# Performance work log

Hardware: AMD Instinct MI355X
Metric: run time of the kernel (lower is better)

Reference implementation:

```python
import jax, jax.numpy as jnp
import numpy as np

N, IN_DIM, H, L, NH, LAT = 4096, 16, 128, 4, 8, 16
HD = H // NH
FF = 2 * H
DR_THR = 0.2
LN_EPS = 1e-5


def _ln(x, s, b):
    m = x.mean(-1, keepdims=True)
    v = ((x - m) ** 2).mean(-1, keepdims=True)
    return (x - m) * jax.lax.rsqrt(v + LN_EPS) * s + b


def compute_dr_mask(x_raw):
    eta = x_raw[:, 1] * (2.62 - (-2.62)) + (-2.62)
    phi = x_raw[:, 2] * (3.1416 - (-3.1416)) + (-3.1416)
    deta = eta[:, None] - eta[None, :]
    dphi = phi[:, None] - phi[None, :]
    dphi = jnp.arctan2(jnp.sin(dphi), jnp.cos(dphi))
    dr = jnp.sqrt(deta ** 2 + dphi ** 2)
    return jnp.where(dr <= DR_THR, 0.0, -jnp.inf).astype(jnp.float32)


def setup_inputs() -> dict:
    key = jax.random.key(0)
    ks = jax.random.split(key, 32)
    g = lambda i, shape, s=0.02: (jax.random.normal(ks[i], shape, dtype=jnp.float32) * s)
    inp = {
        'x_raw': jax.random.uniform(ks[0], (N, IN_DIM), dtype=jnp.float32),
        'batch': jnp.zeros((N,), dtype=jnp.int64) if jax.config.read('jax_enable_x64') else jnp.zeros((N,), dtype=jnp.int32),
        'in_w': g(1, (H, IN_DIM), 0.1), 'in_b': jnp.zeros((H,), jnp.float32),
        'ln1_s': jnp.ones((L, H), jnp.float32), 'ln1_b': jnp.zeros((L, H), jnp.float32),
        'qkv_w': g(2, (L, 3 * H, H)), 'qkv_b': jnp.zeros((L, 3 * H), jnp.float32),
        'ao_w': g(3, (L, H, H)), 'ao_b': jnp.zeros((L, H), jnp.float32),
        'ln2_s': jnp.ones((L, H), jnp.float32), 'ln2_b': jnp.zeros((L, H), jnp.float32),
        'f1_w': g(4, (L, FF, H)), 'f1_b': jnp.zeros((L, FF), jnp.float32),
        'f2_w': g(5, (L, H, FF)), 'f2_b': jnp.zeros((L, H), jnp.float32),
        'lat1_w': g(6, (H, H), 0.08), 'lat1_b': jnp.zeros((H,), jnp.float32),
        'lat2_w': g(7, (LAT, H), 0.08), 'lat2_b': jnp.zeros((LAT,), jnp.float32),
        'b1_w': g(8, (H // 2, H), 0.08), 'b1_b': jnp.zeros((H // 2,), jnp.float32),
        'b2_w': g(9, (1, H // 2), 0.008), 'b2_b': jnp.full((1,), -3.0, jnp.float32),
    }
    return inp


def reference(x_raw, batch, in_w, in_b, ln1_s, ln1_b, qkv_w, qkv_b, ao_w, ao_b,
              ln2_s, ln2_b, f1_w, f1_b, f2_w, f2_b,
              lat1_w, lat1_b, lat2_w, lat2_b, b1_w, b1_b, b2_w, b2_b):
    mask = jax.lax.stop_gradient(compute_dr_mask(x_raw))  # [N, N] additive mask
    x = x_raw @ in_w.T + in_b  # [N, H]
    scale = 1.0 / jnp.sqrt(jnp.float32(HD))
    for l in range(L):  # norm_first TransformerEncoderLayer, eval mode (no dropout)
        h = _ln(x, ln1_s[l], ln1_b[l])
        qkv = h @ qkv_w[l].T + qkv_b[l]
        q, k, v = [t.reshape(N, NH, HD) for t in jnp.split(qkv, 3, axis=-1)]
        scores = jnp.einsum('qhd,khd->hqk', q, k) * scale + mask[None]
        attn = jax.nn.softmax(scores, axis=-1)
        o = jnp.einsum('hqk,khd->qhd', attn, v).reshape(N, H)
        x = x + o @ ao_w[l].T + ao_b[l]
        h2 = _ln(x, ln2_s[l], ln2_b[l])
        x = x + jax.nn.relu(h2 @ f1_w[l].T + f1_b[l]) @ f2_w[l].T + f2_b[l]
    lat = jax.nn.relu(x @ lat1_w.T + lat1_b) @ lat2_w.T + lat2_b  # [N, LAT]
    lat = lat / jnp.maximum(jnp.linalg.norm(lat, axis=-1, keepdims=True), 1e-12)
    beta = jax.nn.sigmoid(jax.nn.relu(x @ b1_w.T + b1_b) @ b2_w.T + b2_b)
    beta = jnp.clip(beta, 1e-6, 1 - 1e-6)  # [N, 1]
    return beta, lat
```

## Files before the change

kernel.cpp:

```cpp
#include <hip/hip_runtime.h>
#include <hip/hip_bf16.h>

typedef unsigned short u16;
typedef short short8_t __attribute__((ext_vector_type(8)));
typedef float floatx4 __attribute__((ext_vector_type(4)));

constexpr int NT = 4096, H = 128, CAP = 64;
constexpr int GRID = 256, BLK = 512, GSTRIDE = GRID * BLK;
constexpr int NGRP = 8, GRPSZ = GRID / NGRP;

constexpr int OFF_QKV  = 0;
constexpr int OFF_AO   = 196608;
constexpr int OFF_F1   = 262144;
constexpr int OFF_F2   = 393216;
constexpr int OFF_LAT1 = 524288;
constexpr int OFF_B1   = 540672;
constexpr int OFF_LAT2 = 548864;
constexpr int W_TOTAL  = 550912;

__device__ __forceinline__ float bfu(u16 u) { return __uint_as_float(((unsigned)u) << 16); }
__device__ __forceinline__ u16 f2bf(float f) {
  unsigned u = __float_as_uint(f);
  u += 0x7fffu + ((u >> 16) & 1u);
  return (u16)(u >> 16);
}
__device__ __forceinline__ void unpack8(uint4 u, float* f) {
  f[0] = __uint_as_float(u.x << 16); f[1] = __uint_as_float(u.x & 0xffff0000u);
  f[2] = __uint_as_float(u.y << 16); f[3] = __uint_as_float(u.y & 0xffff0000u);
  f[4] = __uint_as_float(u.z << 16); f[5] = __uint_as_float(u.z & 0xffff0000u);
  f[6] = __uint_as_float(u.w << 16); f[7] = __uint_as_float(u.w & 0xffff0000u);
}
__device__ __forceinline__ short8_t cvt8(const float* bp) {
  const float4 f0 = *(const float4*)bp, f1 = *(const float4*)(bp + 4);
  short8_t r;
  r[0] = (short)f2bf(f0.x); r[1] = (short)f2bf(f0.y);
  r[2] = (short)f2bf(f0.z); r[3] = (short)f2bf(f0.w);
  r[4] = (short)f2bf(f1.x); r[5] = (short)f2bf(f1.y);
  r[6] = (short)f2bf(f1.z); r[7] = (short)f2bf(f1.w);
  return r;
}

__device__ __forceinline__ void st64(unsigned long long* p, unsigned long long v) {
  __hip_atomic_store(p, v, __ATOMIC_RELAXED, __HIP_MEMORY_SCOPE_AGENT);
}
__device__ __forceinline__ void st16(u16* p, u16 v) {
  __hip_atomic_store(p, v, __ATOMIC_RELAXED, __HIP_MEMORY_SCOPE_AGENT);
}

__device__ __forceinline__ void gridbar(int* bar, int grp, int e) {
  __syncthreads();
  if (threadIdx.x == 0) {
    asm volatile("" ::: "memory");
    int* root = bar;
    int* gcnt = bar + 16 + 16 * grp;
    const int old = __hip_atomic_fetch_add(gcnt, 1, __ATOMIC_RELAXED,
                                           __HIP_MEMORY_SCOPE_AGENT);
    if (old == GRPSZ * e - 1)
      __hip_atomic_fetch_add(root, 1, __ATOMIC_RELAXED, __HIP_MEMORY_SCOPE_AGENT);
    while (__hip_atomic_load(root, __ATOMIC_RELAXED, __HIP_MEMORY_SCOPE_AGENT) < NGRP * e)
      __builtin_amdgcn_s_sleep(2);
    asm volatile("" ::: "memory");
  }
  __syncthreads();
}

struct Prm {
  const float *xr, *in_w, *in_b, *ln1_s, *ln1_b, *qkv_w, *qkv_b, *ao_w, *ao_b,
              *ln2_s, *ln2_b, *f1_w, *f1_b, *f2_w, *f2_b, *lat1_w, *lat1_b,
              *lat2_w, *lat2_b, *b1_w, *b1_b, *b2_w, *b2_b;
  u16* W; u16* QKV[4]; int* bar; float* out;
};

__global__ __launch_bounds__(BLK, 2) void fused_kernel(Prm p) {
  const int t = threadIdx.x, bid = blockIdx.x;
  const int lane = t & 63, w = t >> 6;
  const int lr = lane & 15, quad = lane >> 4;
  const int gtid = bid * BLK + t;
  const int r0 = bid * 16;
  const int grp = bid >> 5;
  const floatx4 FZ = {0.f, 0.f, 0.f, 0.f};
  int bar_k = 0;

  __shared__ float Xs[16][132];
  __shared__ int NIs[16][CAP];
  __shared__ int NCs[16];
  __shared__ union {
    unsigned long long words[8][64];
    struct { u16 A16[16][152]; u16 FF1[16][280]; } g;
    u16 QS[16][384];
  } sm;

  auto stage_x = [&](const float* sc, const float* bi, bool do_ln) {
    const int r = t >> 5, j0 = (t & 31) * 4;
    const float4 xv = *(const float4*)&Xs[r][j0];
    float v0 = xv.x, v1 = xv.y, v2 = xv.z, v3 = xv.w;
    if (do_ln) {
      float s = v0 + v1 + v2 + v3;
      float ss = v0 * v0 + v1 * v1 + v2 * v2 + v3 * v3;
#pragma unroll
      for (int off = 1; off <= 16; off <<= 1) {
        s += __shfl_xor(s, off); ss += __shfl_xor(ss, off);
      }
      const float mean = s * (1.f / 128.f);
      const float rstd = rsqrtf(ss * (1.f / 128.f) - mean * mean + 1e-5f);
      v0 = (v0 - mean) * rstd * sc[j0]     + bi[j0];
      v1 = (v1 - mean) * rstd * sc[j0 + 1] + bi[j0 + 1];
      v2 = (v2 - mean) * rstd * sc[j0 + 2] + bi[j0 + 2];
      v3 = (v3 - mean) * rstd * sc[j0 + 3] + bi[j0 + 3];
    }
    uint2 pk;
    pk.x = (unsigned)f2bf(v0) | ((unsigned)f2bf(v1) << 16);
    pk.y = (unsigned)f2bf(v2) | ((unsigned)f2bf(v3) << 16);
    *(uint2*)&sm.g.A16[r][j0] = pk;
  };

  for (int i = 49152 + gtid; i < W_TOTAL; i += GSTRIDE) {
    float v;
    if      (i < OFF_AO)   v = p.qkv_w[i];
    else if (i < OFF_F1)   v = p.ao_w[i - OFF_AO];
    else if (i < OFF_F2)   v = p.f1_w[i - OFF_F1];
    else if (i < OFF_LAT1) v = p.f2_w[i - OFF_F2];
    else if (i < OFF_B1)   v = p.lat1_w[i - OFF_LAT1];
    else if (i < OFF_LAT2) v = p.b1_w[i - OFF_B1];
    else                   v = p.lat2_w[i - OFF_LAT2];
    st16(&p.W[i], f2bf(v));
  }
  for (int i = t; i < 16 * H; i += BLK) {
    const int r = i >> 7, c = i & 127;
    const float* xp = p.xr + (size_t)(r0 + r) * 16;
    const float* wp = p.in_w + c * 16;
    float acc = p.in_b[c];
#pragma unroll
    for (int k = 0; k < 16; ++k) acc += xp[k] * wp[k];
    Xs[r][c] = acc;
  }
  for (int uu = 0; uu < 2; ++uu) {
    const int q0 = r0 + uu * 8;
    double qe[8], qp_[8];
#pragma unroll
    for (int j = 0; j < 8; ++j) {
      qe[j]  = (double)p.xr[(q0 + j) * 16 + 1] * 5.24 - 2.62;
      qp_[j] = (double)p.xr[(q0 + j) * 16 + 2] * 6.2832 - 3.1416;
    }
    for (int c = 0; c < 8; ++c) {
      const int k = c * 512 + t;
      const double ke = (double)p.xr[k * 16 + 1] * 5.24 - 2.62;
      const double kp = (double)p.xr[k * 16 + 2] * 6.2832 - 3.1416;
#pragma unroll
      for (int j = 0; j < 8; ++j) {
        const double de = qe[j] - ke;
        double dp = qp_[j] - kp;
        dp -= 6.283185307179586 * rint(dp * 0.15915494309189535);
        const unsigned long long bm = __ballot((de * de + dp * dp) <= 0.04);
        if (lane == 0) sm.words[j][c * 8 + w] = bm;
      }
    }
    __syncthreads();
    {
      unsigned long long m = sm.words[w][lane];
      const int cnt = __popcll(m);
      int incl = cnt;
#pragma unroll
      for (int off = 1; off < 64; off <<= 1) {
        const int n = __shfl_up(incl, off);
        if (lane >= off) incl += n;
      }
      int pos = incl - cnt;
      const int lq = uu * 8 + w;
      const int kbase = (lane >> 3) * 512 + (lane & 7) * 64;
      while (m) {
        const int b = __builtin_ctzll(m);
        m &= m - 1;
        if (pos < CAP) NIs[lq][pos] = kbase + b;
        ++pos;
      }
      if (lane == 63) NCs[lq] = incl > CAP ? CAP : incl;
    }
    __syncthreads();
  }
  stage_x(p.ln1_s, p.ln1_b, true);
  __syncthreads();
  {
    const int c0 = w * 48;
    floatx4 a0 = FZ, a1 = FZ, a2 = FZ;
#pragma unroll
    for (int k0 = 0; k0 < 128; k0 += 32) {
      short8_t a  = *(const short8_t*)&sm.g.A16[lr][k0 + quad * 8];
      short8_t b0 = cvt8(&p.qkv_w[(size_t)(c0 + lr) * 128 + k0 + quad * 8]);
      short8_t b1 = cvt8(&p.qkv_w[(size_t)(c0 + 16 + lr) * 128 + k0 + quad * 8]);
      short8_t b2 = cvt8(&p.qkv_w[(size_t)(c0 + 32 + lr) * 128 + k0 + quad * 8]);
      a0 = __builtin_amdgcn_mfma_f32_16x16x32_bf16(a, b0, a0, 0, 0, 0);
      a1 = __builtin_amdgcn_mfma_f32_16x16x32_bf16(a, b1, a1, 0, 0, 0);
      a2 = __builtin_amdgcn_mfma_f32_16x16x32_bf16(a, b2, a2, 0, 0, 0);
    }
    __syncthreads();
#pragma unroll
    for (int r = 0; r < 4; ++r) {
      const int row = quad * 4 + r;
      sm.QS[row][c0 + lr]      = f2bf(a0[r] + p.qkv_b[c0 + lr]);
      sm.QS[row][c0 + 16 + lr] = f2bf(a1[r] + p.qkv_b[c0 + 16 + lr]);
      sm.QS[row][c0 + 32 + lr] = f2bf(a2[r] + p.qkv_b[c0 + 32 + lr]);
    }
    __syncthreads();
    unsigned long long* d64 = (unsigned long long*)(p.QKV[0] + (size_t)r0 * 384);
    const unsigned long long* s64 = (const unsigned long long*)&sm.QS[0][0];
    for (int j = t; j < 1536; j += BLK) st64(&d64[j], s64[j]);
  }
  gridbar(p.bar, grp, ++bar_k);

  for (int l = 0; l < 4; ++l) {
    const u16* __restrict__ qsrc = p.QKV[l];
    u16* __restrict__ qdst = (l < 3) ? p.QKV[l + 1] : nullptr;

    {
      const int pr = t >> 2, sub = t & 3;
      const int lq = pr >> 3, h = pr & 7;
      const u16* qp = qsrc + (size_t)(r0 + lq) * 384 + h * 16;
      float qv[16];
      { uint4 a = *(const uint4*)qp, b = *(const uint4*)(qp + 8);
        unpack8(a, qv); unpack8(b, qv + 8); }
#pragma unroll
      for (int d = 0; d < 16; ++d) qv[d] *= 0.25f;
      float o[16];
#pragma unroll
      for (int d = 0; d < 16; ++d) o[d] = 0.f;
      float se = 0.f;
      const int cnt = NCs[lq];
      for (int i = sub; i < cnt; i += 4) {
        const int nb = NIs[lq][i];
        const u16* kp = qsrc + (size_t)nb * 384 + 128 + h * 16;
        float kv[16], vv[16];
        { uint4 a = *(const uint4*)kp;         uint4 b = *(const uint4*)(kp + 8);
          unpack8(a, kv); unpack8(b, kv + 8); }
        { uint4 a = *(const uint4*)(kp + 128); uint4 b = *(const uint4*)(kp + 136);
          unpack8(a, vv); unpack8(b, vv + 8); }
        float s0 = 0.f, s1 = 0.f, s2 = 0.f, s3 = 0.f;
#pragma unroll
        for (int d = 0; d < 16; d += 4) {
          s0 += qv[d] * kv[d];         s1 += qv[d + 1] * kv[d + 1];
          s2 += qv[d + 2] * kv[d + 2]; s3 += qv[d + 3] * kv[d + 3];
        }
        const float e = __expf((s0 + s1) + (s2 + s3));
        se += e;
#pragma unroll
        for (int d = 0; d < 16; ++d) o[d] += e * vv[d];
      }
#pragma unroll
      for (int d = 0; d < 16; ++d) o[d] += __shfl_xor(o[d], 1);
      se += __shfl_xor(se, 1);
#pragma unroll
      for (int d = 0; d < 16; ++d) o[d] += __shfl_xor(o[d], 2);
      se += __shfl_xor(se, 2);
      if (sub == 0) {
        const float inv = 1.f / se;
        uint4 w0, w1;
        w0.x = (unsigned)f2bf(o[0] * inv)  | ((unsigned)f2bf(o[1] * inv) << 16);
        w0.y = (unsigned)f2bf(o[2] * inv)  | ((unsigned)f2bf(o[3] * inv) << 16);
        w0.z = (unsigned)f2bf(o[4] * inv)  | ((unsigned)f2bf(o[5] * inv) << 16);
        w0.w = (unsigned)f2bf(o[6] * inv)  | ((unsigned)f2bf(o[7] * inv) << 16);
        w1.x = (unsigned)f2bf(o[8] * inv)  | ((unsigned)f2bf(o[9] * inv) << 16);
        w1.y = (unsigned)f2bf(o[10] * inv) | ((unsigned)f2bf(o[11] * inv) << 16);
        w1.z = (unsigned)f2bf(o[12] * inv) | ((unsigned)f2bf(o[13] * inv) << 16);
        w1.w = (unsigned)f2bf(o[14] * inv) | ((unsigned)f2bf(o[15] * inv) << 16);
        *(uint4*)&sm.g.A16[lq][h * 16]     = w0;
        *(uint4*)&sm.g.A16[lq][h * 16 + 8] = w1;
      }
    }
    __syncthreads();
    {
      const u16* Bw = p.W + OFF_AO + l * 16384;
      const float* ab = p.ao_b + l * 128;
      const int col = w * 16 + lr;
      floatx4 acc = FZ;
#pragma unroll
      for (int k0 = 0; k0 < 128; k0 += 32) {
        short8_t a = *(const short8_t*)&sm.g.A16[lr][k0 + quad * 8];
        short8_t b = *(const short8_t*)&Bw[(size_t)col * 128 + k0 + quad * 8];
        acc = __builtin_amdgcn_mfma_f32_16x16x32_bf16(a, b, acc, 0, 0, 0);
      }
      const float bv = ab[col];
#pragma unroll
      for (int r = 0; r < 4; ++r)
        Xs[quad * 4 + r][col] += acc[r] + bv;
    }
    __syncthreads();
    stage_x(p.ln2_s + l * 128, p.ln2_b + l * 128, true);
    __syncthreads();
    {
      const u16* Bw = p.W + OFF_F1 + l * 32768;
      const float* fb = p.f1_b + l * 256;
      const int c0 = w * 32;
      floatx4 a0 = FZ, a1 = FZ;
#pragma unroll
      for (int k0 = 0; k0 < 128; k0 += 32) {
        short8_t a  = *(const short8_t*)&sm.g.A16[lr][k0 + quad * 8];
        short8_t b0 = *(const short8_t*)&Bw[(size_t)(c0 + lr) * 128 + k0 + quad * 8];
        short8_t b1 = *(const short8_t*)&Bw[(size_t)(c0 + 16 + lr) * 128 + k0 + quad * 8];
        a0 = __builtin_amdgcn_mfma_f32_16x16x32_bf16(a, b0, a0, 0, 0, 0);
        a1 = __builtin_amdgcn_mfma_f32_16x16x32_bf16(a, b1, a1, 0, 0, 0);
      }
#pragma unroll
      for (int r = 0; r < 4; ++r) {
        const int row = quad * 4 + r;
        sm.g.FF1[row][c0 + lr]      = f2bf(fmaxf(a0[r] + fb[c0 + lr], 0.f));
        sm.g.FF1[row][c0 + 16 + lr] = f2bf(fmaxf(a1[r] + fb[c0 + 16 + lr], 0.f));
      }
    }
    __syncthreads();
    {
      const u16* Bw = p.W + OFF_F2 + l * 32768;
      const float* fb = p.f2_b + l * 128;
      const int col = w * 16 + lr;
      floatx4 acc = FZ;
#pragma unroll
      for (int k0 = 0; k0 < 256; k0 += 32) {
        short8_t a = *(const short8_t*)&sm.g.FF1[lr][k0 + quad * 8];
        short8_t b = *(const short8_t*)&Bw[(size_t)col * 256 + k0 + quad * 8];
        acc = __builtin_amdgcn_mfma_f32_16x16x32_bf16(a, b, acc, 0, 0, 0);
      }
      const float bv = fb[col];
#pragma unroll
      for (int r = 0; r < 4; ++r)
        Xs[quad * 4 + r][col] += acc[r] + bv;
    }
    __syncthreads();
    if (l < 3) {
      stage_x(p.ln1_s + (l + 1) * 128, p.ln1_b + (l + 1) * 128, true);
      __syncthreads();
      {
        const u16* Bw = p.W + OFF_QKV + (l + 1) * 49152;
        const float* qb = p.qkv_b + (l + 1) * 384;
        const int c0 = w * 48;
        floatx4 a0 = FZ, a1 = FZ, a2 = FZ;
#pragma unroll
        for (int k0 = 0; k0 < 128; k0 += 32) {
          short8_t a  = *(const short8_t*)&sm.g.A16[lr][k0 + quad * 8];
          short8_t b0 = *(const short8_t*)&Bw[(size_t)(c0 + lr) * 128 + k0 + quad * 8];
          short8_t b1 = *(const short8_t*)&Bw[(size_t)(c0 + 16 + lr) * 128 + k0 + quad * 8];
          short8_t b2 = *(const short8_t*)&Bw[(size_t)(c0 + 32 + lr) * 128 + k0 + quad * 8];
          a0 = __builtin_amdgcn_mfma_f32_16x16x32_bf16(a, b0, a0, 0, 0, 0);
          a1 = __builtin_amdgcn_mfma_f32_16x16x32_bf16(a, b1, a1, 0, 0, 0);
          a2 = __builtin_amdgcn_mfma_f32_16x16x32_bf16(a, b2, a2, 0, 0, 0);
        }
        __syncthreads();
#pragma unroll
        for (int r = 0; r < 4; ++r) {
          const int row = quad * 4 + r;
          sm.QS[row][c0 + lr]      = f2bf(a0[r] + qb[c0 + lr]);
          sm.QS[row][c0 + 16 + lr] = f2bf(a1[r] + qb[c0 + 16 + lr]);
          sm.QS[row][c0 + 32 + lr] = f2bf(a2[r] + qb[c0 + 32 + lr]);
        }
        __syncthreads();
        unsigned long long* d64 = (unsigned long long*)(qdst + (size_t)r0 * 384);
        const unsigned long long* s64 = (const unsigned long long*)&sm.QS[0][0];
        for (int j = t; j < 1536; j += BLK) st64(&d64[j], s64[j]);
      }
      gridbar(p.bar, grp, ++bar_k);
    } else {
      stage_x(nullptr, nullptr, false);
      __syncthreads();
      {
        const int c0 = w * 32;
        if (c0 < 192) {
          const u16* Bw = p.W + OFF_LAT1;
          floatx4 a0 = FZ, a1 = FZ;
#pragma unroll
          for (int k0 = 0; k0 < 128; k0 += 32) {
            short8_t a  = *(const short8_t*)&sm.g.A16[lr][k0 + quad * 8];
            short8_t b0 = *(const short8_t*)&Bw[(size_t)(c0 + lr) * 128 + k0 + quad * 8];
            short8_t b1 = *(const short8_t*)&Bw[(size_t)(c0 + 16 + lr) * 128 + k0 + quad * 8];
            a0 = __builtin_amdgcn_mfma_f32_16x16x32_bf16(a, b0, a0, 0, 0, 0);
            a1 = __builtin_amdgcn_mfma_f32_16x16x32_bf16(a, b1, a1, 0, 0, 0);
          }
          const int cA = c0 + lr, cB = c0 + 16 + lr;
          const float bA = cA < 128 ? p.lat1_b[cA] : p.b1_b[cA - 128];
          const float bB = cB < 128 ? p.lat1_b[cB] : p.b1_b[cB - 128];
#pragma unroll
          for (int r = 0; r < 4; ++r) {
            const int row = quad * 4 + r;
            sm.g.FF1[row][cA] = f2bf(fmaxf(a0[r] + bA, 0.f));
            sm.g.FF1[row][cB] = f2bf(fmaxf(a1[r] + bB, 0.f));
          }
        }
      }
      __syncthreads();
      if (t < 256) {
        const int r = t >> 4, c = t & 15;
        float acc = p.lat2_b[c];
        const u16* gw = p.W + OFF_LAT2 + c * 128;
        for (int k = 0; k < 128; ++k) acc += bfu(sm.g.FF1[r][k]) * bfu(gw[k]);
        float ss = acc * acc;
        ss += __shfl_xor(ss, 1); ss += __shfl_xor(ss, 2);
        ss += __shfl_xor(ss, 4); ss += __shfl_xor(ss, 8);
        p.out[NT + (size_t)(r0 + r) * 16 + c] = acc / fmaxf(sqrtf(ss), 1e-12f);
        float v = 0.f;
#pragma unroll
        for (int i = 0; i < 4; ++i)
          v += bfu(sm.g.FF1[r][128 + c * 4 + i]) * p.b2_w[c * 4 + i];
        v += __shfl_xor(v, 1); v += __shfl_xor(v, 2);
        v += __shfl_xor(v, 4); v += __shfl_xor(v, 8);
        if (c == 0) {
          v += p.b2_b[0];
          const float beta = 1.f / (1.f + __expf(-v));
          p.out[r0 + r] = fminf(fmaxf(beta, 1e-6f), 1.f - 1e-6f);
        }
      }
    }
  }
}

extern "C" void kernel_launch(void* const* d_in, const int* in_sizes, int n_in,
                              void* d_out, int out_size, void* d_ws, size_t ws_size,
                              hipStream_t stream) {
  Prm prm;
  prm.xr    = (const float*)d_in[0];
  prm.in_w  = (const float*)d_in[2];  prm.in_b  = (const float*)d_in[3];
  prm.ln1_s = (const float*)d_in[4];  prm.ln1_b = (const float*)d_in[5];
  prm.qkv_w = (const float*)d_in[6];  prm.qkv_b = (const float*)d_in[7];
  prm.ao_w  = (const float*)d_in[8];  prm.ao_b  = (const float*)d_in[9];
  prm.ln2_s = (const float*)d_in[10]; prm.ln2_b = (const float*)d_in[11];
  prm.f1_w  = (const float*)d_in[12]; prm.f1_b  = (const float*)d_in[13];
  prm.f2_w  = (const float*)d_in[14]; prm.f2_b  = (const float*)d_in[15];
  prm.lat1_w= (const float*)d_in[16]; prm.lat1_b= (const float*)d_in[17];
  prm.lat2_w= (const float*)d_in[18]; prm.lat2_b= (const float*)d_in[19];
  prm.b1_w  = (const float*)d_in[20]; prm.b1_b  = (const float*)d_in[21];
  prm.b2_w  = (const float*)d_in[22]; prm.b2_b  = (const float*)d_in[23];
  prm.out   = (float*)d_out;

  char* pw = (char*)d_ws;
  prm.W    = (u16*)pw;   pw += ((size_t)W_TOTAL * 2 + 255) & ~(size_t)255;
  for (int i = 0; i < 4; ++i) { prm.QKV[i] = (u16*)pw; pw += (size_t)NT * 384 * 2; }
  prm.bar  = (int*)pw;   pw += 2048;

  hipMemsetAsync(prm.bar, 0, 2048, stream);
  fused_kernel<<<GRID, BLK, 0, stream>>>(prm);
}
```

Before: 192.7 us.

## Template rows-per-block and launch 512 blocks of 8 rows when occupancy allows

Makes the number of query rows per block a template parameter and launches 512 blocks of 8 rows instead of 256 blocks of 16, provided the occupancy query reports at least two resident blocks per CU. The aim is to fill more CUs and give each row more attention threads (SUB=8 neighbour lanes instead of 4). In exchange the grid barriers have more participants, MFMA tiles are half idle (16-row tiles holding 8 rows), weights are re-read per block twice as often, and launch_bounds is dropped, which may raise register use.

```diff
diff --git a/kernel.cpp b/kernel.cpp
--- a/kernel.cpp
+++ b/kernel.cpp
@@ -6,8 +6,8 @@
 typedef float floatx4 __attribute__((ext_vector_type(4)));
 
 constexpr int NT = 4096, H = 128, CAP = 64;
-constexpr int GRID = 256, BLK = 512, GSTRIDE = GRID * BLK;
-constexpr int NGRP = 8, GRPSZ = GRID / NGRP;
+constexpr int BLK = 512;
+constexpr int NGRP = 8;
 
 constexpr int OFF_QKV  = 0;
 constexpr int OFF_AO   = 196608;
@@ -47,6 +47,7 @@
   __hip_atomic_store(p, v, __ATOMIC_RELAXED, __HIP_MEMORY_SCOPE_AGENT);
 }
 
+template <int GRPSZ>
 __device__ __forceinline__ void gridbar(int* bar, int grp, int e) {
   __syncthreads();
   if (threadIdx.x == 0) {
@@ -71,47 +72,55 @@
   u16* W; u16* QKV[4]; int* bar; float* out;
 };
 
-__global__ __launch_bounds__(BLK, 2) void fused_kernel(Prm p) {
+template <int NROWS>
+__global__ void fused_kernel(Prm p) {
+  constexpr int GRID_ = NT / NROWS;
+  constexpr int GRPSZ = GRID_ / NGRP;
+  constexpr int GSTRIDE = GRID_ * BLK;
+  constexpr int SUB = BLK / (NROWS * 8);
+
   const int t = threadIdx.x, bid = blockIdx.x;
   const int lane = t & 63, w = t >> 6;
   const int lr = lane & 15, quad = lane >> 4;
   const int gtid = bid * BLK + t;
-  const int r0 = bid * 16;
-  const int grp = bid >> 5;
+  const int r0 = bid * NROWS;
+  const int grp = bid / GRPSZ;
   const floatx4 FZ = {0.f, 0.f, 0.f, 0.f};
   int bar_k = 0;
 
-  __shared__ float Xs[16][132];
-  __shared__ int NIs[16][CAP];
-  __shared__ int NCs[16];
+  __shared__ float Xs[NROWS][132];
+  __shared__ int NIs[NROWS][CAP];
+  __shared__ int NCs[NROWS];
   __shared__ union {
     unsigned long long words[8][64];
     struct { u16 A16[16][152]; u16 FF1[16][280]; } g;
-    u16 QS[16][384];
+    u16 QS[NROWS][384];
   } sm;
 
   auto stage_x = [&](const float* sc, const float* bi, bool do_ln) {
-    const int r = t >> 5, j0 = (t & 31) * 4;
-    const float4 xv = *(const float4*)&Xs[r][j0];
-    float v0 = xv.x, v1 = xv.y, v2 = xv.z, v3 = xv.w;
-    if (do_ln) {
-      float s = v0 + v1 + v2 + v3;
-      float ss = v0 * v0 + v1 * v1 + v2 * v2 + v3 * v3;
-#pragma unroll
-      for (int off = 1; off <= 16; off <<= 1) {
-        s += __shfl_xor(s, off); ss += __shfl_xor(ss, off);
-      }
-      const float mean = s * (1.f / 128.f);
-      const float rstd = rsqrtf(ss * (1.f / 128.f) - mean * mean + 1e-5f);
-      v0 = (v0 - mean) * rstd * sc[j0]     + bi[j0];
-      v1 = (v1 - mean) * rstd * sc[j0 + 1] + bi[j0 + 1];
-      v2 = (v2 - mean) * rstd * sc[j0 + 2] + bi[j0 + 2];
-      v3 = (v3 - mean) * rstd * sc[j0 + 3] + bi[j0 + 3];
-    }
-    uint2 pk;
-    pk.x = (unsigned)f2bf(v0) | ((unsigned)f2bf(v1) << 16);
-    pk.y = (unsigned)f2bf(v2) | ((unsigned)f2bf(v3) << 16);
-    *(uint2*)&sm.g.A16[r][j0] = pk;
+    if (t < NROWS * 32) {
+      const int r = t >> 5, j0 = (t & 31) * 4;
+      const float4 xv = *(const float4*)&Xs[r][j0];
+      float v0 = xv.x, v1 = xv.y, v2 = xv.z, v3 = xv.w;
+      if (do_ln) {
+        float s = v0 + v1 + v2 + v3;
+        float ss = v0 * v0 + v1 * v1 + v2 * v2 + v3 * v3;
+#pragma unroll
+        for (int off = 1; off <= 16; off <<= 1) {
+          s += __shfl_xor(s, off); ss += __shfl_xor(ss, off);
+        }
+        const float mean = s * (1.f / 128.f);
+        const float rstd = rsqrtf(ss * (1.f / 128.f) - mean * mean + 1e-5f);
+        v0 = (v0 - mean) * rstd * sc[j0]     + bi[j0];
+        v1 = (v1 - mean) * rstd * sc[j0 + 1] + bi[j0 + 1];
+        v2 = (v2 - mean) * rstd * sc[j0 + 2] + bi[j0 + 2];
+        v3 = (v3 - mean) * rstd * sc[j0 + 3] + bi[j0 + 3];
+      }
+      uint2 pk;
+      pk.x = (unsigned)f2bf(v0) | ((unsigned)f2bf(v1) << 16);
+      pk.y = (unsigned)f2bf(v2) | ((unsigned)f2bf(v3) << 16);
+      *(uint2*)&sm.g.A16[r][j0] = pk;
+    }
   };
 
   for (int i = 49152 + gtid; i < W_TOTAL; i += GSTRIDE) {
@@ -125,7 +134,7 @@
     else                   v = p.lat2_w[i - OFF_LAT2];
     st16(&p.W[i], f2bf(v));
   }
-  for (int i = t; i < 16 * H; i += BLK) {
+  for (int i = t; i < NROWS * H; i += BLK) {
     const int r = i >> 7, c = i & 127;
     const float* xp = p.xr + (size_t)(r0 + r) * 16;
     const float* wp = p.in_w + c * 16;
@@ -134,7 +143,7 @@
     for (int k = 0; k < 16; ++k) acc += xp[k] * wp[k];
     Xs[r][c] = acc;
   }
-  for (int uu = 0; uu < 2; ++uu) {
+  for (int uu = 0; uu < NROWS / 8; ++uu) {
     const int q0 = r0 + uu * 8;
     double qe[8], qp_[8];
 #pragma unroll
@@ -197,23 +206,25 @@
 #pragma unroll
     for (int r = 0; r < 4; ++r) {
       const int row = quad * 4 + r;
-      sm.QS[row][c0 + lr]      = f2bf(a0[r] + p.qkv_b[c0 + lr]);
-      sm.QS[row][c0 + 16 + lr] = f2bf(a1[r] + p.qkv_b[c0 + 16 + lr]);
-      sm.QS[row][c0 + 32 + lr] = f2bf(a2[r] + p.qkv_b[c0 + 32 + lr]);
+      if (row < NROWS) {
+        sm.QS[row][c0 + lr]      = f2bf(a0[r] + p.qkv_b[c0 + lr]);
+        sm.QS[row][c0 + 16 + lr] = f2bf(a1[r] + p.qkv_b[c0 + 16 + lr]);
+        sm.QS[row][c0 + 32 + lr] = f2bf(a2[r] + p.qkv_b[c0 + 32 + lr]);
+      }
     }
     __syncthreads();
     unsigned long long* d64 = (unsigned long long*)(p.QKV[0] + (size_t)r0 * 384);
     const unsigned long long* s64 = (const unsigned long long*)&sm.QS[0][0];
-    for (int j = t; j < 1536; j += BLK) st64(&d64[j], s64[j]);
-  }
-  gridbar(p.bar, grp, ++bar_k);
+    for (int j = t; j < NROWS * 96; j += BLK) st64(&d64[j], s64[j]);
+  }
+  gridbar<GRPSZ>(p.bar, grp, ++bar_k);
 
   for (int l = 0; l < 4; ++l) {
     const u16* __restrict__ qsrc = p.QKV[l];
     u16* __restrict__ qdst = (l < 3) ? p.QKV[l + 1] : nullptr;
 
     {
-      const int pr = t >> 2, sub = t & 3;
+      const int pr = t / SUB, sub = t % SUB;
       const int lq = pr >> 3, h = pr & 7;
       const u16* qp = qsrc + (size_t)(r0 + lq) * 384 + h * 16;
       float qv[16];
@@ -226,7 +237,7 @@
       for (int d = 0; d < 16; ++d) o[d] = 0.f;
       float se = 0.f;
       const int cnt = NCs[lq];
-      for (int i = sub; i < cnt; i += 4) {
+      for (int i = sub; i < cnt; i += SUB) {
         const int nb = NIs[lq][i];
         const u16* kp = qsrc + (size_t)nb * 384 + 128 + h * 16;
         float kv[16], vv[16];
@@ -246,11 +257,11 @@
         for (int d = 0; d < 16; ++d) o[d] += e * vv[d];
       }
 #pragma unroll
-      for (int d = 0; d < 16; ++d) o[d] += __shfl_xor(o[d], 1);
-      se += __shfl_xor(se, 1);
-#pragma unroll
-      for (int d = 0; d < 16; ++d) o[d] += __shfl_xor(o[d], 2);
-      se += __shfl_xor(se, 2);
+      for (int off = 1; off < SUB; off <<= 1) {
+#pragma unroll
+        for (int d = 0; d < 16; ++d) o[d] += __shfl_xor(o[d], off);
+        se += __shfl_xor(se, off);
+      }
       if (sub == 0) {
         const float inv = 1.f / se;
         uint4 w0, w1;
@@ -280,8 +291,10 @@
       }
       const float bv = ab[col];
 #pragma unroll
-      for (int r = 0; r < 4; ++r)
-        Xs[quad * 4 + r][col] += acc[r] + bv;
+      for (int r = 0; r < 4; ++r) {
+        const int row = quad * 4 + r;
+        if (row < NROWS) Xs[row][col] += acc[r] + bv;
+      }
     }
     __syncthreads();
     stage_x(p.ln2_s + l * 128, p.ln2_b + l * 128, true);
@@ -302,8 +315,10 @@
 #pragma unroll
       for (int r = 0; r < 4; ++r) {
         const int row = quad * 4 + r;
-        sm.g.FF1[row][c0 + lr]      = f2bf(fmaxf(a0[r] + fb[c0 + lr], 0.f));
-        sm.g.FF1[row][c0 + 16 + lr] = f2bf(fmaxf(a1[r] + fb[c0 + 16 + lr], 0.f));
+        if (row < NROWS) {
+          sm.g.FF1[row][c0 + lr]      = f2bf(fmaxf(a0[r] + fb[c0 + lr], 0.f));
+          sm.g.FF1[row][c0 + 16 + lr] = f2bf(fmaxf(a1[r] + fb[c0 + 16 + lr], 0.f));
+        }
       }
     }
     __syncthreads();
@@ -320,8 +335,10 @@
       }
       const float bv = fb[col];
 #pragma unroll
-      for (int r = 0; r < 4; ++r)
-        Xs[quad * 4 + r][col] += acc[r] + bv;
+      for (int r = 0; r < 4; ++r) {
+        const int row = quad * 4 + r;
+        if (row < NROWS) Xs[row][col] += acc[r] + bv;
+      }
     }
     __syncthreads();
     if (l < 3) {
@@ -346,16 +363,18 @@
 #pragma unroll
         for (int r = 0; r < 4; ++r) {
           const int row = quad * 4 + r;
-          sm.QS[row][c0 + lr]      = f2bf(a0[r] + qb[c0 + lr]);
-          sm.QS[row][c0 + 16 + lr] = f2bf(a1[r] + qb[c0 + 16 + lr]);
-          sm.QS[row][c0 + 32 + lr] = f2bf(a2[r] + qb[c0 + 32 + lr]);
+          if (row < NROWS) {
+            sm.QS[row][c0 + lr]      = f2bf(a0[r] + qb[c0 + lr]);
+            sm.QS[row][c0 + 16 + lr] = f2bf(a1[r] + qb[c0 + 16 + lr]);
+            sm.QS[row][c0 + 32 + lr] = f2bf(a2[r] + qb[c0 + 32 + lr]);
+          }
         }
         __syncthreads();
         unsigned long long* d64 = (unsigned long long*)(qdst + (size_t)r0 * 384);
         const unsigned long long* s64 = (const unsigned long long*)&sm.QS[0][0];
-        for (int j = t; j < 1536; j += BLK) st64(&d64[j], s64[j]);
-      }
-      gridbar(p.bar, grp, ++bar_k);
+        for (int j = t; j < NROWS * 96; j += BLK) st64(&d64[j], s64[j]);
+      }
+      gridbar<GRPSZ>(p.bar, grp, ++bar_k);
     } else {
       stage_x(nullptr, nullptr, false);
       __syncthreads();
@@ -378,13 +397,15 @@
 #pragma unroll
           for (int r = 0; r < 4; ++r) {
             const int row = quad * 4 + r;
-            sm.g.FF1[row][cA] = f2bf(fmaxf(a0[r] + bA, 0.f));
-            sm.g.FF1[row][cB] = f2bf(fmaxf(a1[r] + bB, 0.f));
+            if (row < NROWS) {
+              sm.g.FF1[row][cA] = f2bf(fmaxf(a0[r] + bA, 0.f));
+              sm.g.FF1[row][cB] = f2bf(fmaxf(a1[r] + bB, 0.f));
+            }
           }
         }
       }
       __syncthreads();
-      if (t < 256) {
+      if (t < NROWS * 16) {
         const int r = t >> 4, c = t & 15;
         float acc = p.lat2_b[c];
         const u16* gw = p.W + OFF_LAT2 + c * 128;
@@ -432,6 +453,13 @@
   for (int i = 0; i < 4; ++i) { prm.QKV[i] = (u16*)pw; pw += (size_t)NT * 384 * 2; }
   prm.bar  = (int*)pw;   pw += 2048;
 
+  int maxb8 = 0;
+  hipOccupancyMaxActiveBlocksPerMultiprocessor(&maxb8, fused_kernel<8>, BLK, 0);
+
   hipMemsetAsync(prm.bar, 0, 2048, stream);
-  fused_kernel<<<GRID, BLK, 0, stream>>>(prm);
-}
+  if (maxb8 >= 2) {
+    fused_kernel<8><<<NT / 8, BLK, 0, stream>>>(prm);
+  } else {
+    fused_kernel<16><<<NT / 16, BLK, 0, stream>>>(prm);
+  }
+}
```

Result: no change. 196.5 us (+2.0%).

## Keep Q in registers from shared memory, store only K/V globally, prefetch neighbors

Applied to the files above, without the earlier changes.

Q for each block's own rows is now read straight from shared memory into registers right after the QKV projection, so only K and V (256 columns instead of 384) are written to the global scratch buffers. This cuts global store traffic per layer and removes the Q reload after the grid barrier. The sparse attention loop also software-pipelines the K/V gather, loading the next neighbor's K/V while computing on the current one. The cost is higher register pressure from the prefetch buffers and the persistent qv array under launch bounds of 2 blocks per CU.

```diff
diff --git a/kernel.cpp b/kernel.cpp
--- a/kernel.cpp
+++ b/kernel.cpp
@@ -68,7 +68,7 @@
   const float *xr, *in_w, *in_b, *ln1_s, *ln1_b, *qkv_w, *qkv_b, *ao_w, *ao_b,
               *ln2_s, *ln2_b, *f1_w, *f1_b, *f2_w, *f2_b, *lat1_w, *lat1_b,
               *lat2_w, *lat2_b, *b1_w, *b1_b, *b2_w, *b2_b;
-  u16* W; u16* QKV[4]; int* bar; float* out;
+  u16* W; u16* KV[4]; int* bar; float* out;
 };
 
 __global__ __launch_bounds__(BLK, 2) void fused_kernel(Prm p) {
@@ -81,6 +81,10 @@
   const floatx4 FZ = {0.f, 0.f, 0.f, 0.f};
   int bar_k = 0;
 
+  const int pr = t >> 2, sub = t & 3;
+  const int lq = pr >> 3, h = pr & 7;
+  float qv[16];
+
   __shared__ float Xs[16][132];
   __shared__ int NIs[16][CAP];
   __shared__ int NCs[16];
@@ -112,6 +116,14 @@
     pk.x = (unsigned)f2bf(v0) | ((unsigned)f2bf(v1) << 16);
     pk.y = (unsigned)f2bf(v2) | ((unsigned)f2bf(v3) << 16);
     *(uint2*)&sm.g.A16[r][j0] = pk;
+  };
+
+  auto load_qv = [&]() {
+    const u16* qp = &sm.QS[lq][h * 16];
+    uint4 a = *(const uint4*)qp, b = *(const uint4*)(qp + 8);
+    unpack8(a, qv); unpack8(b, qv + 8);
+#pragma unroll
+    for (int d = 0; d < 16; ++d) qv[d] *= 0.25f;
   };
 
   for (int i = 49152 + gtid; i < W_TOTAL; i += GSTRIDE) {
@@ -166,15 +178,15 @@
         if (lane >= off) incl += n;
       }
       int pos = incl - cnt;
-      const int lq = uu * 8 + w;
+      const int lq2 = uu * 8 + w;
       const int kbase = (lane >> 3) * 512 + (lane & 7) * 64;
       while (m) {
         const int b = __builtin_ctzll(m);
         m &= m - 1;
-        if (pos < CAP) NIs[lq][pos] = kbase + b;
+        if (pos < CAP) NIs[lq2][pos] = kbase + b;
         ++pos;
       }
-      if (lane == 63) NCs[lq] = incl > CAP ? CAP : incl;
+      if (lane == 63) NCs[lq2] = incl > CAP ? CAP : incl;
     }
     __syncthreads();
   }
@@ -202,38 +214,43 @@
       sm.QS[row][c0 + 32 + lr] = f2bf(a2[r] + p.qkv_b[c0 + 32 + lr]);
     }
     __syncthreads();
-    unsigned long long* d64 = (unsigned long long*)(p.QKV[0] + (size_t)r0 * 384);
-    const unsigned long long* s64 = (const unsigned long long*)&sm.QS[0][0];
-    for (int j = t; j < 1536; j += BLK) st64(&d64[j], s64[j]);
+    load_qv();
+    unsigned long long* d64 = (unsigned long long*)(p.KV[0] + (size_t)r0 * 256);
+    for (int j = t; j < 16 * 64; j += BLK) {
+      const int row = j >> 6;
+      st64(&d64[j], ((const unsigned long long*)&sm.QS[row][128])[j & 63]);
+    }
   }
   gridbar(p.bar, grp, ++bar_k);
 
   for (int l = 0; l < 4; ++l) {
-    const u16* __restrict__ qsrc = p.QKV[l];
-    u16* __restrict__ qdst = (l < 3) ? p.QKV[l + 1] : nullptr;
+    const u16* __restrict__ kvsrc = p.KV[l];
+    u16* __restrict__ kvdst = (l < 3) ? p.KV[l + 1] : nullptr;
 
     {
-      const int pr = t >> 2, sub = t & 3;
-      const int lq = pr >> 3, h = pr & 7;
-      const u16* qp = qsrc + (size_t)(r0 + lq) * 384 + h * 16;
-      float qv[16];
-      { uint4 a = *(const uint4*)qp, b = *(const uint4*)(qp + 8);
-        unpack8(a, qv); unpack8(b, qv + 8); }
-#pragma unroll
-      for (int d = 0; d < 16; ++d) qv[d] *= 0.25f;
       float o[16];
 #pragma unroll
       for (int d = 0; d < 16; ++d) o[d] = 0.f;
       float se = 0.f;
       const int cnt = NCs[lq];
-      for (int i = sub; i < cnt; i += 4) {
-        const int nb = NIs[lq][i];
-        const u16* kp = qsrc + (size_t)nb * 384 + 128 + h * 16;
+      int i = sub;
+      uint4 ck0, ck1, cv0, cv1;
+      if (i < cnt) {
+        const u16* kp = kvsrc + (size_t)NIs[lq][i] * 256 + h * 16;
+        ck0 = *(const uint4*)kp;         ck1 = *(const uint4*)(kp + 8);
+        cv0 = *(const uint4*)(kp + 128); cv1 = *(const uint4*)(kp + 136);
+      }
+      while (i < cnt) {
+        const int inx = i + 4;
+        uint4 nk0, nk1, nv0, nv1;
+        if (inx < cnt) {
+          const u16* kp = kvsrc + (size_t)NIs[lq][inx] * 256 + h * 16;
+          nk0 = *(const uint4*)kp;         nk1 = *(const uint4*)(kp + 8);
+          nv0 = *(const uint4*)(kp + 128); nv1 = *(const uint4*)(kp + 136);
+        }
         float kv[16], vv[16];
-        { uint4 a = *(const uint4*)kp;         uint4 b = *(const uint4*)(kp + 8);
-          unpack8(a, kv); unpack8(b, kv + 8); }
-        { uint4 a = *(const uint4*)(kp + 128); uint4 b = *(const uint4*)(kp + 136);
-          unpack8(a, vv); unpack8(b, vv + 8); }
+        unpack8(ck0, kv); unpack8(ck1, kv + 8);
+        unpack8(cv0, vv); unpack8(cv1, vv + 8);
         float s0 = 0.f, s1 = 0.f, s2 = 0.f, s3 = 0.f;
 #pragma unroll
         for (int d = 0; d < 16; d += 4) {
@@ -244,6 +261,8 @@
         se += e;
 #pragma unroll
         for (int d = 0; d < 16; ++d) o[d] += e * vv[d];
+        ck0 = nk0; ck1 = nk1; cv0 = nv0; cv1 = nv1;
+        i = inx;
       }
 #pragma unroll
       for (int d = 0; d < 16; ++d) o[d] += __shfl_xor(o[d], 1);
@@ -351,9 +370,12 @@
           sm.QS[row][c0 + 32 + lr] = f2bf(a2[r] + qb[c0 + 32 + lr]);
         }
         __syncthreads();
-        unsigned long long* d64 = (unsigned long long*)(qdst + (size_t)r0 * 384);
-        const unsigned long long* s64 = (const unsigned long long*)&sm.QS[0][0];
-        for (int j = t; j < 1536; j += BLK) st64(&d64[j], s64[j]);
+        load_qv();
+        unsigned long long* d64 = (unsigned long long*)(kvdst + (size_t)r0 * 256);
+        for (int j = t; j < 16 * 64; j += BLK) {
+          const int row = j >> 6;
+          st64(&d64[j], ((const unsigned long long*)&sm.QS[row][128])[j & 63]);
+        }
       }
       gridbar(p.bar, grp, ++bar_k);
     } else {
@@ -429,7 +451,7 @@
 
   char* pw = (char*)d_ws;
   prm.W    = (u16*)pw;   pw += ((size_t)W_TOTAL * 2 + 255) & ~(size_t)255;
-  for (int i = 0; i < 4; ++i) { prm.QKV[i] = (u16*)pw; pw += (size_t)NT * 384 * 2; }
+  for (int i = 0; i < 4; ++i) { prm.KV[i] = (u16*)pw; pw += (size_t)NT * 256 * 2; }
   prm.bar  = (int*)pw;   pw += 2048;
 
   hipMemsetAsync(prm.bar, 0, 2048, stream);
```

Result: no change. 193.7 us (+0.5%).
